# Optimization experiments

Measured on AMD Instinct MI355X. Metric: run time of the kernel, lower is better.

## Reference

```python
import jax, jax.numpy as jnp
import numpy as np

B, N, T, F, D, R, K, L, E = 4, 2000, 50, 10, 64, 8, 16, 3, 32


def setup_inputs() -> dict:
    key = jax.random.key(0)
    ks = jax.random.split(key, 12)
    rn = lambda k, shape, sc: (jax.random.normal(k, shape, jnp.float32) * sc)
    return {
        "X": jax.random.normal(ks[0], (B, N, T, F), jnp.float32),
        "neighbors": jax.random.randint(ks[1], (B, R, N, K), 0, N + 1),
        "gru_W": rn(ks[2], (F, 3 * D), 0.1),
        "gru_U": rn(ks[3], (D, 3 * D), 0.1),
        "gru_b": jnp.zeros((2, 3 * D), jnp.float32),
        "rel_emb": rn(ks[4], (R, E), 0.1),
        "proj_W": rn(ks[5], (R, D, D), 0.05),
        "proj_b": jnp.zeros((R, D), jnp.float32),
        "satt_W": rn(ks[6], (R, 2 * D + E), 0.05),
        "satt_b": jnp.zeros((R,), jnp.float32),
        "ratt_W": rn(ks[7], (2 * D + E,), 0.05),
        "ratt_b": jnp.zeros((), jnp.float32),
        "pred_W": rn(ks[8], (D, L), 0.05),
        "pred_b": jnp.zeros((L,), jnp.float32),
    }


def leaky(x):  # tf.nn.leaky_relu default alpha=0.2
    return jnp.where(x >= 0, x, 0.2 * x)


def gru(x, W, U, b):
    # Keras GRU (reset_after=True), gate order [z, r, h]. x: (M, T, F)
    xp = x @ W + b[0]                      # (M, T, 3D) input projections, precomputed
    h0 = jnp.zeros((x.shape[0], U.shape[0]), x.dtype)

    def step(h, xt):
        rec = h @ U + b[1]
        xz, xr, xh = jnp.split(xt, 3, axis=-1)
        rz, rr, rh = jnp.split(rec, 3, axis=-1)
        z = jax.nn.sigmoid(xz + rz)
        r = jax.nn.sigmoid(xr + rr)
        hh = jnp.tanh(xh + r * rh)
        return z * h + (1.0 - z) * hh, None

    h, _ = jax.lax.scan(step, h0, jnp.swapaxes(xp, 0, 1))
    return h


def reference(X, neighbors, gru_W, gru_U, gru_b, rel_emb, proj_W, proj_b,
              satt_W, satt_b, ratt_W, ratt_b, pred_W, pred_b):
    b, n, t, f = X.shape
    d = gru_U.shape[0]

    # --- GRU feature extraction (dropout inactive at inference) ---
    node = gru(X.reshape(b * n, t, f), gru_W, gru_U, gru_b).reshape(b, n, d)
    padded = jnp.concatenate([jnp.zeros((b, 1, d), node.dtype), node], axis=1)  # (B, N+1, D)

    # --- per-relation neighbor gather + projection ---
    neigh_raw = jax.vmap(lambda nf, idx: nf[idx])(padded, neighbors)            # (B, R, N, K, D)
    neigh = leaky(jnp.einsum('brnkd,rde->brnke', neigh_raw, proj_W)
                  + proj_b[None, :, None, None, :])                              # (B, R, N, K, D)

    cur = node                                                                   # (B, N, D)

    # --- state attention: Dense(1) on concat[cur, neigh, rel_emb], split weights ---
    w_cur, w_ngh, w_rel = satt_W[:, :d], satt_W[:, d:2 * d], satt_W[:, 2 * d:]
    s_cur = jnp.einsum('bnd,rd->brn', cur, w_cur)                                # (B, R, N)
    s_ngh = jnp.einsum('brnkd,rd->brnk', neigh, w_ngh)                           # (B, R, N, K)
    s_rel = jnp.einsum('re,re->r', rel_emb, w_rel) + satt_b                      # (R,)
    scores = leaky(s_cur[:, :, :, None] + s_ngh + s_rel[None, :, None, None])
    scores = scores + jnp.where(neighbors == 0, -1e9, 0.0).astype(scores.dtype)  # mask padding node
    att = jax.nn.softmax(scores, axis=-1)                                        # over K
    rel_rep = jnp.einsum('brnk,brnkd->brnd', att, neigh)                         # (B, R, N, D)

    # --- relation attention ---
    rep_t = jnp.transpose(rel_rep, (0, 2, 1, 3))                                 # (B, N, R, D)
    r_cur, r_rep, r_emb = ratt_W[:d], ratt_W[d:2 * d], ratt_W[2 * d:]
    rs = leaky(jnp.einsum('bnd,d->bn', cur, r_cur)[:, :, None]
               + jnp.einsum('bnrd,d->bnr', rep_t, r_rep)
               + (rel_emb @ r_emb)[None, None, :] + ratt_b)                      # (B, N, R)
    ratt = jax.nn.softmax(rs, axis=-1)
    agg = jnp.einsum('bnr,bnrd->bnd', ratt, rep_t)
    updated = cur + agg

    # --- prediction head ---
    return jax.nn.softmax(updated @ pred_W + pred_b)
```

## Files before the change

### kernel.cpp

```cpp
#include <hip/hip_runtime.h>
#include <hip/hip_bf16.h>
#include <cstddef>

constexpr int cB=4, cN=2000, cT=50, cF=10, cD=64, cR=8, cK=16, cE=32;
constexpr int NODES = cB*cN;
constexpr int N1    = cN+1;
constexpr int ROWS2 = cB*N1;

#define DEV static __device__ __forceinline__

typedef __attribute__((ext_vector_type(8))) short bf16x8;
typedef __attribute__((ext_vector_type(4))) float f32x4;
typedef __attribute__((ext_vector_type(4))) int   i32x4;

DEV float leaky(float x){ return fmaxf(x, 0.2f*x); }
DEV float wsumall(float v){
  v += __shfl_xor(v,32,64); v += __shfl_xor(v,16,64); v += __shfl_xor(v,8,64);
  v += __shfl_xor(v,4,64);  v += __shfl_xor(v,2,64);  v += __shfl_xor(v,1,64);
  return v;
}
DEV unsigned fu(float f){ return __float_as_uint(f); }
DEV float hif(float f){ return __uint_as_float(fu(f) & 0xFFFF0000u); }
DEV unsigned rne16(float f){
  unsigned u = fu(f);
  return (u + 0x7FFFu + ((u>>16)&1u)) >> 16;
}
DEV bf16x8 pack4(unsigned a, unsigned b, unsigned c2, unsigned d){
  union { i32x4 i; bf16x8 h; } u;
  u.i = (i32x4){(int)a,(int)b,(int)c2,(int)d};
  return u.h;
}
DEV unsigned PLO(unsigned x, unsigned y){ return __builtin_amdgcn_perm(y, x, 0x05040100u); }
DEV unsigned PHI(unsigned x, unsigned y){ return __builtin_amdgcn_perm(y, x, 0x07060302u); }
DEV f32x4 MF(bf16x8 a, bf16x8 b, f32x4 c){
  return __builtin_amdgcn_mfma_f32_16x16x32_bf16(a, b, c, 0, 0, 0);
}
DEV float bfu(unsigned short u){ return __uint_as_float(((unsigned)u)<<16); }

__global__ __launch_bounds__(256, 2) void k_gru(const float* __restrict__ X,
    const float* __restrict__ gW, const float* __restrict__ gU,
    const float* __restrict__ gb, const float* __restrict__ pW,
    const float* __restrict__ pb, const float* __restrict__ sattW,
    float* __restrict__ node, unsigned short* __restrict__ actb,
    float* __restrict__ sng2)
{
  __shared__ unsigned sH[2][1024];

  const int tid  = threadIdx.x;
  const int lane = tid & 63;
  const int w    = tid >> 6;
  const int c    = lane & 15;
  const int kg   = lane >> 4;
  const int nb   = (int)blockIdx.x * 16;
  const int col  = 16*w + c;
  const int bb   = nb / cN;

  bf16x8 BUhi[2][3], BUlo[2][3], BX[3];
  #pragma unroll
  for (int s=0;s<2;++s){
    #pragma unroll
    for (int cls=0; cls<3; ++cls){
      const int n = cls*64 + col;
      unsigned hi[4], lo[4];
      #pragma unroll
      for (int p=0;p<4;++p){
        float u0 = gU[(s*32 + kg*8 + 2*p    )*192 + n];
        float u1 = gU[(s*32 + kg*8 + 2*p + 1)*192 + n];
        hi[p] = (fu(u0)>>16) | (fu(u1) & 0xFFFF0000u);
        lo[p] = rne16(u0 - hif(u0)) | (rne16(u1 - hif(u1)) << 16);
      }
      BUhi[s][cls] = pack4(hi[0],hi[1],hi[2],hi[3]);
      BUlo[s][cls] = pack4(lo[0],lo[1],lo[2],lo[3]);
    }
  }
  #pragma unroll
  for (int cls=0; cls<3; ++cls){
    const int n = cls*64 + col;
    unsigned wd[4];
    #pragma unroll
    for (int p=0;p<4;++p){
      int f = kg*4 + p;
      unsigned v = (f < cF) ? rne16(gW[f*192 + n]) : 0u;
      wd[p] = v | (v << 16);
    }
    BX[cls] = pack4(wd[0],wd[1],wd[2],wd[3]);
  }

  const float bz  = gb[col]      + gb[192+col];
  const float br  = gb[64+col]   + gb[256+col];
  const float bh0 = gb[128+col];
  const float bh1 = gb[320+col];

  for (int i2 = tid; i2 < 1024; i2 += 256) sH[0][i2] = 0u;
  f32x4 ho = {0.f,0.f,0.f,0.f};
  __syncthreads();

  float xc[4], xn[4];
  const float* Xb = X + (size_t)(nb + c)*cT*cF;
  {
    #pragma unroll
    for (int p=0;p<4;++p){ int f = 4*kg+p; xc[p] = (f < cF) ? Xb[0*cF + f] : 0.f; }
    #pragma unroll
    for (int p=0;p<4;++p){ int f = 4*kg+p; xn[p] = (f < cF) ? Xb[1*cF + f] : 0.f; }
  }

  const unsigned sw  = (unsigned)((c&7)<<2);
  const unsigned rb0 = (unsigned)(c*64 + kg*8);

  for (int t = 0; t < cT; ++t){
    unsigned xw[4];
    #pragma unroll
    for (int p=0;p<4;++p)
      xw[p] = (fu(xc[p])>>16) | (rne16(xc[p] - hif(xc[p])) << 16);
    bf16x8 xf = pack4(xw[0],xw[1],xw[2],xw[3]);

    #pragma unroll
    for (int p=0;p<4;++p) xc[p] = xn[p];
    {
      int tn = (t+2 < cT) ? t+2 : cT-1;
      #pragma unroll
      for (int p=0;p<4;++p){ int f = 4*kg+p; xn[p] = (f < cF) ? Xb[(size_t)tn*cF + f] : 0.f; }
    }

    const unsigned* sr = sH[t & 1];
    i32x4 qa = *(const i32x4*)(sr + ((rb0 +  0) ^ sw));
    i32x4 qb = *(const i32x4*)(sr + ((rb0 +  4) ^ sw));
    i32x4 qc = *(const i32x4*)(sr + ((rb0 + 32) ^ sw));
    i32x4 qd = *(const i32x4*)(sr + ((rb0 + 36) ^ sw));
    bf16x8 hh0 = pack4(PLO(qa[0],qa[1]), PLO(qa[2],qa[3]), PLO(qb[0],qb[1]), PLO(qb[2],qb[3]));
    bf16x8 hl0 = pack4(PHI(qa[0],qa[1]), PHI(qa[2],qa[3]), PHI(qb[0],qb[1]), PHI(qb[2],qb[3]));
    bf16x8 hh1 = pack4(PLO(qc[0],qc[1]), PLO(qc[2],qc[3]), PLO(qd[0],qd[1]), PLO(qd[2],qd[3]));
    bf16x8 hl1 = pack4(PHI(qc[0],qc[1]), PHI(qc[2],qc[3]), PHI(qd[0],qd[1]), PHI(qd[2],qd[3]));

    f32x4 aZ  = {bz,bz,bz,bz};
    f32x4 aR  = {br,br,br,br};
    f32x4 aHc = {bh1,bh1,bh1,bh1};
    f32x4 aXh = {bh0,bh0,bh0,bh0};
    aZ  = MF(xf, BX[0], aZ);
    aR  = MF(xf, BX[1], aR);
    aXh = MF(xf, BX[2], aXh);
    aZ  = MF(hh0, BUhi[0][0], aZ);  aZ  = MF(hh1, BUhi[1][0], aZ);
    aR  = MF(hh0, BUhi[0][1], aR);  aR  = MF(hh1, BUhi[1][1], aR);
    aHc = MF(hh0, BUhi[0][2], aHc); aHc = MF(hh1, BUhi[1][2], aHc);
    aZ  = MF(hl0, BUhi[0][0], aZ);  aZ  = MF(hl1, BUhi[1][0], aZ);
    aR  = MF(hl0, BUhi[0][1], aR);  aR  = MF(hl1, BUhi[1][1], aR);
    aHc = MF(hl0, BUhi[0][2], aHc); aHc = MF(hl1, BUhi[1][2], aHc);
    aZ  = MF(hh0, BUlo[0][0], aZ);  aZ  = MF(hh1, BUlo[1][0], aZ);
    aR  = MF(hh0, BUlo[0][1], aR);  aR  = MF(hh1, BUlo[1][1], aR);
    aHc = MF(hh0, BUlo[0][2], aHc); aHc = MF(hh1, BUlo[1][2], aHc);

    unsigned* swr = sH[(t & 1) ^ 1];
    #pragma unroll
    for (int reg=0; reg<4; ++reg){
      float z  = __builtin_amdgcn_rcpf(1.0f + __expf(-aZ[reg]));
      float r  = __builtin_amdgcn_rcpf(1.0f + __expf(-aR[reg]));
      float pre = __builtin_fmaf(r, aHc[reg], aXh[reg]);
      float th = 1.0f - 2.0f*__builtin_amdgcn_rcpf(__expf(2.0f*pre) + 1.0f);
      float hn = __builtin_fmaf(z, ho[reg]-th, th);
      ho[reg] = hn;
      unsigned val = (fu(hn)>>16) | (rne16(hn - hif(hn)) << 16);
      int nodei = kg*4 + reg;
      swr[((unsigned)(nodei*64 + col)) ^ ((unsigned)((nodei&7)<<2))] = val;
    }
    asm volatile("s_waitcnt lgkmcnt(0)" ::: "memory");
    __builtin_amdgcn_s_barrier();
  }

  #pragma unroll
  for (int reg=0; reg<4; ++reg)
    node[(size_t)(nb + kg*4 + reg)*cD + col] = ho[reg];

  {
    const unsigned* sr = &sH[0][0];
    i32x4 qa = *(const i32x4*)(sr + ((rb0 +  0) ^ sw));
    i32x4 qb = *(const i32x4*)(sr + ((rb0 +  4) ^ sw));
    i32x4 qc = *(const i32x4*)(sr + ((rb0 + 32) ^ sw));
    i32x4 qd = *(const i32x4*)(sr + ((rb0 + 36) ^ sw));
    bf16x8 hh0 = pack4(PLO(qa[0],qa[1]), PLO(qa[2],qa[3]), PLO(qb[0],qb[1]), PLO(qb[2],qb[3]));
    bf16x8 hl0 = pack4(PHI(qa[0],qa[1]), PHI(qa[2],qa[3]), PHI(qb[0],qb[1]), PHI(qb[2],qb[3]));
    bf16x8 hh1 = pack4(PLO(qc[0],qc[1]), PLO(qc[2],qc[3]), PLO(qd[0],qd[1]), PLO(qd[2],qd[3]));
    bf16x8 hl1 = pack4(PHI(qc[0],qc[1]), PHI(qc[2],qc[3]), PHI(qd[0],qd[1]), PHI(qd[2],qd[3]));

    const int qbase = nb + bb + 1;
    #pragma unroll
    for (int r2=0; r2<2; ++r2){
      const int r = 2*w + r2;
      const float* Pr = pW + (size_t)r*cD*cD;
      bf16x8 PB[4][2];
      float pbv[4], wnv[4];
      #pragma unroll
      for (int cb=0; cb<4; ++cb){
        const int e = 16*cb + c;
        #pragma unroll
        for (int s=0;s<2;++s){
          unsigned wd[4];
          #pragma unroll
          for (int p=0;p<4;++p){
            int k0 = s*32 + kg*8 + 2*p;
            wd[p] = rne16(Pr[(size_t)k0*cD + e]) | (rne16(Pr[(size_t)(k0+1)*cD + e]) << 16);
          }
          PB[cb][s] = pack4(wd[0],wd[1],wd[2],wd[3]);
        }
        pbv[cb] = pb[r*cD + e];
        wnv[cb] = sattW[r*(2*cD+cE) + cD + e];
      }
      float sp[4] = {0.f,0.f,0.f,0.f};
      #pragma unroll
      for (int cb=0; cb<4; ++cb){
        f32x4 acc = {pbv[cb],pbv[cb],pbv[cb],pbv[cb]};
        acc = MF(hh0, PB[cb][0], acc); acc = MF(hh1, PB[cb][1], acc);
        acc = MF(hl0, PB[cb][0], acc); acc = MF(hl1, PB[cb][1], acc);
        #pragma unroll
        for (int reg=0; reg<4; ++reg){
          float o = leaky(acc[reg]);
          int qrow = qbase + kg*4 + reg;
          actb[((size_t)r*ROWS2 + qrow)*cD + 16*cb + c] = (unsigned short)rne16(o);
          sp[reg] = __builtin_fmaf(o, wnv[cb], sp[reg]);
        }
      }
      #pragma unroll
      for (int reg=0; reg<4; ++reg){
        float s2 = sp[reg];
        s2 += __shfl_xor(s2,1,64); s2 += __shfl_xor(s2,2,64);
        s2 += __shfl_xor(s2,4,64); s2 += __shfl_xor(s2,8,64);
        if (c == 0) sng2[(size_t)r*ROWS2 + qbase + kg*4 + reg] = s2;
      }
    }
  }

  if ((blockIdx.x % (cN/16)) == 0){
    #pragma unroll
    for (int r2=0; r2<2; ++r2){
      const int r = 2*w + r2;
      float v0 = leaky(pb[r*cD + lane]);
      float wv = sattW[r*(2*cD+cE) + cD + lane];
      actb[((size_t)r*ROWS2 + (size_t)bb*N1)*cD + lane] = (unsigned short)rne16(v0);
      float s2 = wsumall(v0 * wv);
      if (lane == 0) sng2[(size_t)r*ROWS2 + (size_t)bb*N1] = s2;
    }
  }
}

__global__ __launch_bounds__(256) void k_attn(const float* __restrict__ node,
    const int* __restrict__ nbrs, const float* __restrict__ sattW,
    const float* __restrict__ sattb, const float* __restrict__ rattW,
    const float* __restrict__ rattb, const float* __restrict__ predW,
    const float* __restrict__ predb, const float* __restrict__ relemb,
    const unsigned short* __restrict__ actb, const float* __restrict__ sng2,
    float* __restrict__ out)
{
  __shared__ float sSA[cR][cD];
  __shared__ float sSrel[cR], sRremb[cR];
  __shared__ float sAtt[4][cR][cK];
  __shared__ int   sOff[4][cR][cK];
  const int tid = threadIdx.x;
  for (int i=tid; i<cR*cD; i+=256) sSA[i>>6][i&63] = sattW[(i>>6)*(2*cD+cE) + (i&63)];
  if (tid < 64){
    int r = tid >> 3, j0 = (tid & 7)*4;
    float a = 0.f, b2 = 0.f;
    #pragma unroll
    for (int j=0;j<4;++j){
      float re = relemb[r*cE + j0 + j];
      a  += re * sattW[r*(2*cD+cE) + 2*cD + j0 + j];
      b2 += re * rattW[2*cD + j0 + j];
    }
    a  += __shfl_xor(a,1,64);  a  += __shfl_xor(a,2,64);  a  += __shfl_xor(a,4,64);
    b2 += __shfl_xor(b2,1,64); b2 += __shfl_xor(b2,2,64); b2 += __shfl_xor(b2,4,64);
    if ((tid & 7) == 0){ sSrel[r] = a + sattb[r]; sRremb[r] = b2; }
  }
  __syncthreads();

  const int wave = tid >> 6, lane = tid & 63;
  const int gn = (int)blockIdx.x*4 + wave;
  const int b = __builtin_amdgcn_readfirstlane(gn / cN);
  const int n = __builtin_amdgcn_readfirstlane(gn % cN);

  const float cur = node[(size_t)gn*cD + lane];

  float scr[8];
  #pragma unroll
  for (int r=0; r<8; ++r) scr[r] = wsumall(cur * sSA[r][lane]);

  const int g = lane >> 4, k = lane & 15;
  #pragma unroll
  for (int half=0; half<2; ++half){
    int r = half*4 + g;
    float sc0 = half==0 ? (g==0?scr[0]:g==1?scr[1]:g==2?scr[2]:scr[3])
                        : (g==0?scr[4]:g==1?scr[5]:g==2?scr[6]:scr[7]);
    int idx = nbrs[(((size_t)b*cR + r)*cN + n)*cK + k];
    int o = r*ROWS2 + b*N1 + idx;
    float sv = sng2[o];
    float sc = leaky(sc0 + sv + sSrel[r]);
    if (idx == 0) sc -= 1e9f;
    float mx = sc;
    mx = fmaxf(mx, __shfl_xor(mx,1,64)); mx = fmaxf(mx, __shfl_xor(mx,2,64));
    mx = fmaxf(mx, __shfl_xor(mx,4,64)); mx = fmaxf(mx, __shfl_xor(mx,8,64));
    float ex = __expf(sc - mx);
    float sm = ex;
    sm += __shfl_xor(sm,1,64); sm += __shfl_xor(sm,2,64);
    sm += __shfl_xor(sm,4,64); sm += __shfl_xor(sm,8,64);
    sAtt[wave][r][k] = ex/sm;
    sOff[wave][r][k] = o;
  }
  __syncthreads();

  float facc[8];
  #pragma unroll
  for (int r=0; r<8; ++r){
    float a0=0.f, a1=0.f;
    #pragma unroll
    for (int kk=0; kk<cK; kk+=2){
      float w0 = sAtt[wave][r][kk],   w1 = sAtt[wave][r][kk+1];
      int   o0 = sOff[wave][r][kk],   o1 = sOff[wave][r][kk+1];
      a0 += w0 * bfu(actb[(size_t)o0*cD + lane]);
      a1 += w1 * bfu(actb[(size_t)o1*cD + lane]);
    }
    facc[r] = a0 + a1;
  }

  const float rcur = rattW[lane], rrep = rattW[cD + lane];
  const float rb   = rattb[0];
  const float c0 = wsumall(cur * rcur);
  float rs[8];
  #pragma unroll
  for (int r=0; r<8; ++r) rs[r] = leaky(c0 + wsumall(facc[r]*rrep) + sRremb[r] + rb);
  float mx = rs[0];
  #pragma unroll
  for (int r=1; r<8; ++r) mx = fmaxf(mx, rs[r]);
  float es = 0.f; float ratt[8];
  #pragma unroll
  for (int r=0; r<8; ++r){ ratt[r] = __expf(rs[r]-mx); es += ratt[r]; }
  float inv = 1.f/es;
  float agg = 0.f;
  #pragma unroll
  for (int r=0; r<8; ++r) agg += (ratt[r]*inv) * facc[r];
  const float upd = cur + agg;

  float l0 = wsumall(upd * predW[lane*3 + 0]);
  float l1 = wsumall(upd * predW[lane*3 + 1]);
  float l2 = wsumall(upd * predW[lane*3 + 2]);
  if (lane == 0){
    l0 += predb[0]; l1 += predb[1]; l2 += predb[2];
    float m2 = fmaxf(l0, fmaxf(l1, l2));
    float e0 = __expf(l0-m2), e1 = __expf(l1-m2), e2 = __expf(l2-m2);
    float is = 1.f/(e0+e1+e2);
    out[(size_t)gn*3+0] = e0*is;
    out[(size_t)gn*3+1] = e1*is;
    out[(size_t)gn*3+2] = e2*is;
  }
}

extern "C" void kernel_launch(void* const* d_in, const int* in_sizes, int n_in,
                              void* d_out, int out_size, void* d_ws, size_t ws_size,
                              hipStream_t stream)
{
  const float* X      = (const float*)d_in[0];
  const int*   nbrs   = (const int*)  d_in[1];
  const float* gW     = (const float*)d_in[2];
  const float* gU     = (const float*)d_in[3];
  const float* gb     = (const float*)d_in[4];
  const float* relemb = (const float*)d_in[5];
  const float* pW     = (const float*)d_in[6];
  const float* pb     = (const float*)d_in[7];
  const float* sattW  = (const float*)d_in[8];
  const float* sattb  = (const float*)d_in[9];
  const float* rattW  = (const float*)d_in[10];
  const float* rattb  = (const float*)d_in[11];
  const float* predW  = (const float*)d_in[12];
  const float* predb  = (const float*)d_in[13];
  float* out = (float*)d_out;

  float*          node  = (float*)d_ws;
  unsigned short* actb  = (unsigned short*)(node + (size_t)NODES*cD);
  float*          sng2  = (float*)(actb + (size_t)cR*ROWS2*cD);

  k_gru <<<NODES/16, 256, 0, stream>>>(X, gW, gU, gb, pW, pb, sattW,
                                       node, actb, sng2);
  k_attn<<<NODES/4, 256, 0, stream>>>(node, nbrs, sattW, sattb, rattW, rattb,
                                      predW, predb, relemb, actb, sng2, out);
}
```

Baseline: 88.80 us.

## Switch GRU recurrence from split-bf16 MFMA to single fp16 MFMA with folded scales

Replaces the three-pass split-bf16 (hi/lo) recurrent matmul with a single fp16 MFMA per tile. The weights are prescaled by -log2(e) and 2*log2(e) so the sigmoid and tanh can use a raw v_exp_f32, and the input bias is folded into the input MFMA through a constant-1 feature slot. The hidden state shared-memory buffer is halved and the permute/unpack work is removed. This cuts MFMA count and ALU work on the serial 50-step critical path, at the cost of fp16 precision in the hidden state and weights, which could exceed the accuracy tolerance.

```diff
diff --git a/kernel.cpp b/kernel.cpp
--- a/kernel.cpp
+++ b/kernel.cpp
@@ -1,6 +1,7 @@
 #include <hip/hip_runtime.h>
 #include <hip/hip_bf16.h>
 #include <cstddef>
+#include <cstring>
 
 constexpr int cB=4, cN=2000, cT=50, cF=10, cD=64, cR=8, cK=16, cE=32;
 constexpr int NODES = cB*cN;
@@ -9,9 +10,10 @@
 
 #define DEV static __device__ __forceinline__
 
-typedef __attribute__((ext_vector_type(8))) short bf16x8;
-typedef __attribute__((ext_vector_type(4))) float f32x4;
-typedef __attribute__((ext_vector_type(4))) int   i32x4;
+typedef __attribute__((ext_vector_type(8))) short    bf16x8;
+typedef __attribute__((ext_vector_type(8))) _Float16 f16x8;
+typedef __attribute__((ext_vector_type(4))) float    f32x4;
+typedef __attribute__((ext_vector_type(4))) int      i32x4;
 
 DEV float leaky(float x){ return fmaxf(x, 0.2f*x); }
 DEV float wsumall(float v){
@@ -20,22 +22,28 @@
   return v;
 }
 DEV unsigned fu(float f){ return __float_as_uint(f); }
-DEV float hif(float f){ return __uint_as_float(fu(f) & 0xFFFF0000u); }
 DEV unsigned rne16(float f){
   unsigned u = fu(f);
   return (u + 0x7FFFu + ((u>>16)&1u)) >> 16;
 }
-DEV bf16x8 pack4(unsigned a, unsigned b, unsigned c2, unsigned d){
-  union { i32x4 i; bf16x8 h; } u;
+DEV unsigned f16b(float f){
+  _Float16 h = (_Float16)f;
+  unsigned short u; __builtin_memcpy(&u, &h, 2);
+  return (unsigned)u;
+}
+DEV f16x8 packh(unsigned a, unsigned b, unsigned c2, unsigned d){
+  union { i32x4 i; f16x8 h; } u;
   u.i = (i32x4){(int)a,(int)b,(int)c2,(int)d};
   return u.h;
 }
-DEV unsigned PLO(unsigned x, unsigned y){ return __builtin_amdgcn_perm(y, x, 0x05040100u); }
-DEV unsigned PHI(unsigned x, unsigned y){ return __builtin_amdgcn_perm(y, x, 0x07060302u); }
-DEV f32x4 MF(bf16x8 a, bf16x8 b, f32x4 c){
-  return __builtin_amdgcn_mfma_f32_16x16x32_bf16(a, b, c, 0, 0, 0);
+DEV f16x8 asf16(i32x4 v){
+  union { i32x4 i; f16x8 h; } u; u.i = v; return u.h;
+}
+DEV f32x4 MF16(f16x8 a, f16x8 b, f32x4 c){
+  return __builtin_amdgcn_mfma_f32_16x16x32_f16(a, b, c, 0, 0, 0);
 }
 DEV float bfu(unsigned short u){ return __uint_as_float(((unsigned)u)<<16); }
+DEV float ex2(float x){ float r; asm("v_exp_f32 %0, %1" : "=v"(r) : "v"(x)); return r; }
 
 __global__ __launch_bounds__(256, 2) void k_gru(const float* __restrict__ X,
     const float* __restrict__ gW, const float* __restrict__ gU,
@@ -44,7 +52,7 @@
     float* __restrict__ node, unsigned short* __restrict__ actb,
     float* __restrict__ sng2)
 {
-  __shared__ unsigned sH[2][1024];
+  __shared__ unsigned sF[2][512];
 
   const int tid  = threadIdx.x;
   const int lane = tid & 63;
@@ -55,112 +63,108 @@
   const int col  = 16*w + c;
   const int bb   = nb / cN;
 
-  bf16x8 BUhi[2][3], BUlo[2][3], BX[3];
+  const float SZ = -1.4426950408889634f;
+  const float SH =  2.8853900817779268f;
+
+  f16x8 Uf[2][3];
   #pragma unroll
   for (int s=0;s<2;++s){
     #pragma unroll
     for (int cls=0; cls<3; ++cls){
+      const float sc = (cls==2) ? SH : SZ;
       const int n = cls*64 + col;
-      unsigned hi[4], lo[4];
+      unsigned wd[4];
       #pragma unroll
       for (int p=0;p<4;++p){
-        float u0 = gU[(s*32 + kg*8 + 2*p    )*192 + n];
-        float u1 = gU[(s*32 + kg*8 + 2*p + 1)*192 + n];
-        hi[p] = (fu(u0)>>16) | (fu(u1) & 0xFFFF0000u);
-        lo[p] = rne16(u0 - hif(u0)) | (rne16(u1 - hif(u1)) << 16);
-      }
-      BUhi[s][cls] = pack4(hi[0],hi[1],hi[2],hi[3]);
-      BUlo[s][cls] = pack4(lo[0],lo[1],lo[2],lo[3]);
-    }
-  }
+        int d0 = s*32 + kg*8 + 2*p;
+        wd[p] = f16b(sc*gU[d0*192 + n]) | (f16b(sc*gU[(d0+1)*192 + n]) << 16);
+      }
+      Uf[s][cls] = packh(wd[0],wd[1],wd[2],wd[3]);
+    }
+  }
+  const float bzt = SZ*(gb[col] + gb[192+col]);
+  const float brt = SZ*(gb[64+col] + gb[256+col]);
+  const float bh0 = SH* gb[128+col];
+  const float bh1 = SH* gb[320+col];
+  f16x8 BXf[3];
   #pragma unroll
   for (int cls=0; cls<3; ++cls){
+    const float sc = (cls==2) ? SH : SZ;
+    const float bv = (cls==0) ? bzt : (cls==1 ? brt : bh0);
     const int n = cls*64 + col;
     unsigned wd[4];
     #pragma unroll
     for (int p=0;p<4;++p){
       int f = kg*4 + p;
-      unsigned v = (f < cF) ? rne16(gW[f*192 + n]) : 0u;
-      wd[p] = v | (v << 16);
-    }
-    BX[cls] = pack4(wd[0],wd[1],wd[2],wd[3]);
-  }
-
-  const float bz  = gb[col]      + gb[192+col];
-  const float br  = gb[64+col]   + gb[256+col];
-  const float bh0 = gb[128+col];
-  const float bh1 = gb[320+col];
-
-  for (int i2 = tid; i2 < 1024; i2 += 256) sH[0][i2] = 0u;
+      unsigned v = (f < cF) ? f16b(sc*gW[f*192 + n]) : ((f == cF) ? f16b(bv) : 0u);
+      wd[p] = v;
+    }
+    BXf[cls] = packh(wd[0],wd[1],wd[2],wd[3]);
+  }
+
+  for (int i2 = tid; i2 < 512; i2 += 256) sF[0][i2] = 0u;
   f32x4 ho = {0.f,0.f,0.f,0.f};
   __syncthreads();
 
   float xc[4], xn[4];
   const float* Xb = X + (size_t)(nb + c)*cT*cF;
-  {
-    #pragma unroll
-    for (int p=0;p<4;++p){ int f = 4*kg+p; xc[p] = (f < cF) ? Xb[0*cF + f] : 0.f; }
-    #pragma unroll
-    for (int p=0;p<4;++p){ int f = 4*kg+p; xn[p] = (f < cF) ? Xb[1*cF + f] : 0.f; }
-  }
-
-  const unsigned sw  = (unsigned)((c&7)<<2);
-  const unsigned rb0 = (unsigned)(c*64 + kg*8);
+  #pragma unroll
+  for (int p=0;p<4;++p){
+    int f = 4*kg+p;
+    float fill = (f == cF) ? 1.0f : 0.0f;
+    xc[p] = (f < cF) ? Xb[0*cF + f] : fill;
+    xn[p] = (f < cF) ? Xb[1*cF + f] : fill;
+  }
+
+  const unsigned sw2   = (unsigned)((c&7)<<2);
+  const unsigned base0 = ((unsigned)(c*32 + kg*4))      ^ sw2;
+  const unsigned base1 = ((unsigned)(c*32 + 16 + kg*4)) ^ sw2;
+  unsigned hws[4];
+  #pragma unroll
+  for (int reg=0; reg<4; ++reg){
+    int nodei = kg*4 + reg;
+    hws[reg] = (((unsigned)(nodei*32 + (col>>1))) ^ ((unsigned)((nodei&7)<<2)))*2
+               + (unsigned)(col&1);
+  }
+  const f32x4 zq = {0.f,0.f,0.f,0.f};
 
   for (int t = 0; t < cT; ++t){
-    unsigned xw[4];
-    #pragma unroll
-    for (int p=0;p<4;++p)
-      xw[p] = (fu(xc[p])>>16) | (rne16(xc[p] - hif(xc[p])) << 16);
-    bf16x8 xf = pack4(xw[0],xw[1],xw[2],xw[3]);
-
+    f16x8 xf = packh(f16b(xc[0]), f16b(xc[1]), f16b(xc[2]), f16b(xc[3]));
     #pragma unroll
     for (int p=0;p<4;++p) xc[p] = xn[p];
     {
       int tn = (t+2 < cT) ? t+2 : cT-1;
       #pragma unroll
-      for (int p=0;p<4;++p){ int f = 4*kg+p; xn[p] = (f < cF) ? Xb[(size_t)tn*cF + f] : 0.f; }
-    }
-
-    const unsigned* sr = sH[t & 1];
-    i32x4 qa = *(const i32x4*)(sr + ((rb0 +  0) ^ sw));
-    i32x4 qb = *(const i32x4*)(sr + ((rb0 +  4) ^ sw));
-    i32x4 qc = *(const i32x4*)(sr + ((rb0 + 32) ^ sw));
-    i32x4 qd = *(const i32x4*)(sr + ((rb0 + 36) ^ sw));
-    bf16x8 hh0 = pack4(PLO(qa[0],qa[1]), PLO(qa[2],qa[3]), PLO(qb[0],qb[1]), PLO(qb[2],qb[3]));
-    bf16x8 hl0 = pack4(PHI(qa[0],qa[1]), PHI(qa[2],qa[3]), PHI(qb[0],qb[1]), PHI(qb[2],qb[3]));
-    bf16x8 hh1 = pack4(PLO(qc[0],qc[1]), PLO(qc[2],qc[3]), PLO(qd[0],qd[1]), PLO(qd[2],qd[3]));
-    bf16x8 hl1 = pack4(PHI(qc[0],qc[1]), PHI(qc[2],qc[3]), PHI(qd[0],qd[1]), PHI(qd[2],qd[3]));
-
-    f32x4 aZ  = {bz,bz,bz,bz};
-    f32x4 aR  = {br,br,br,br};
+      for (int p=0;p<4;++p){
+        int f = 4*kg+p;
+        float fill = (f == cF) ? 1.0f : 0.0f;
+        xn[p] = (f < cF) ? Xb[(size_t)tn*cF + f] : fill;
+      }
+    }
+
+    const unsigned* sr = sF[t & 1];
+    i32x4 q0 = *(const i32x4*)(sr + base0);
+    i32x4 q1 = *(const i32x4*)(sr + base1);
+    f16x8 ha = asf16(q0), hb = asf16(q1);
+
+    f32x4 aZ  = MF16(xf, BXf[0], zq);
+    f32x4 aR  = MF16(xf, BXf[1], zq);
+    f32x4 aXh = MF16(xf, BXf[2], zq);
     f32x4 aHc = {bh1,bh1,bh1,bh1};
-    f32x4 aXh = {bh0,bh0,bh0,bh0};
-    aZ  = MF(xf, BX[0], aZ);
-    aR  = MF(xf, BX[1], aR);
-    aXh = MF(xf, BX[2], aXh);
-    aZ  = MF(hh0, BUhi[0][0], aZ);  aZ  = MF(hh1, BUhi[1][0], aZ);
-    aR  = MF(hh0, BUhi[0][1], aR);  aR  = MF(hh1, BUhi[1][1], aR);
-    aHc = MF(hh0, BUhi[0][2], aHc); aHc = MF(hh1, BUhi[1][2], aHc);
-    aZ  = MF(hl0, BUhi[0][0], aZ);  aZ  = MF(hl1, BUhi[1][0], aZ);
-    aR  = MF(hl0, BUhi[0][1], aR);  aR  = MF(hl1, BUhi[1][1], aR);
-    aHc = MF(hl0, BUhi[0][2], aHc); aHc = MF(hl1, BUhi[1][2], aHc);
-    aZ  = MF(hh0, BUlo[0][0], aZ);  aZ  = MF(hh1, BUlo[1][0], aZ);
-    aR  = MF(hh0, BUlo[0][1], aR);  aR  = MF(hh1, BUlo[1][1], aR);
-    aHc = MF(hh0, BUlo[0][2], aHc); aHc = MF(hh1, BUlo[1][2], aHc);
-
-    unsigned* swr = sH[(t & 1) ^ 1];
+    aZ  = MF16(ha, Uf[0][0], aZ);  aZ  = MF16(hb, Uf[1][0], aZ);
+    aR  = MF16(ha, Uf[0][1], aR);  aR  = MF16(hb, Uf[1][1], aR);
+    aHc = MF16(ha, Uf[0][2], aHc); aHc = MF16(hb, Uf[1][2], aHc);
+
+    unsigned short* swr = (unsigned short*)sF[(t & 1) ^ 1];
     #pragma unroll
     for (int reg=0; reg<4; ++reg){
-      float z  = __builtin_amdgcn_rcpf(1.0f + __expf(-aZ[reg]));
-      float r  = __builtin_amdgcn_rcpf(1.0f + __expf(-aR[reg]));
-      float pre = __builtin_fmaf(r, aHc[reg], aXh[reg]);
-      float th = 1.0f - 2.0f*__builtin_amdgcn_rcpf(__expf(2.0f*pre) + 1.0f);
-      float hn = __builtin_fmaf(z, ho[reg]-th, th);
+      float z   = __builtin_amdgcn_rcpf(1.0f + ex2(aZ[reg]));
+      float r   = __builtin_amdgcn_rcpf(1.0f + ex2(aR[reg]));
+      float phv = __builtin_fmaf(r, aHc[reg], aXh[reg]);
+      float th  = __builtin_fmaf(-2.0f, __builtin_amdgcn_rcpf(ex2(phv) + 1.0f), 1.0f);
+      float hn  = __builtin_fmaf(z, ho[reg]-th, th);
       ho[reg] = hn;
-      unsigned val = (fu(hn)>>16) | (rne16(hn - hif(hn)) << 16);
-      int nodei = kg*4 + reg;
-      swr[((unsigned)(nodei*64 + col)) ^ ((unsigned)((nodei&7)<<2))] = val;
+      swr[hws[reg]] = (unsigned short)f16b(hn);
     }
     asm volatile("s_waitcnt lgkmcnt(0)" ::: "memory");
     __builtin_amdgcn_s_barrier();
@@ -171,35 +175,30 @@
     node[(size_t)(nb + kg*4 + reg)*cD + col] = ho[reg];
 
   {
-    const unsigned* sr = &sH[0][0];
-    i32x4 qa = *(const i32x4*)(sr + ((rb0 +  0) ^ sw));
-    i32x4 qb = *(const i32x4*)(sr + ((rb0 +  4) ^ sw));
-    i32x4 qc = *(const i32x4*)(sr + ((rb0 + 32) ^ sw));
-    i32x4 qd = *(const i32x4*)(sr + ((rb0 + 36) ^ sw));
-    bf16x8 hh0 = pack4(PLO(qa[0],qa[1]), PLO(qa[2],qa[3]), PLO(qb[0],qb[1]), PLO(qb[2],qb[3]));
-    bf16x8 hl0 = pack4(PHI(qa[0],qa[1]), PHI(qa[2],qa[3]), PHI(qb[0],qb[1]), PHI(qb[2],qb[3]));
-    bf16x8 hh1 = pack4(PLO(qc[0],qc[1]), PLO(qc[2],qc[3]), PLO(qd[0],qd[1]), PLO(qd[2],qd[3]));
-    bf16x8 hl1 = pack4(PHI(qc[0],qc[1]), PHI(qc[2],qc[3]), PHI(qd[0],qd[1]), PHI(qd[2],qd[3]));
+    const unsigned* sr = &sF[0][0];
+    i32x4 q0 = *(const i32x4*)(sr + base0);
+    i32x4 q1 = *(const i32x4*)(sr + base1);
+    f16x8 ha = asf16(q0), hb = asf16(q1);
 
     const int qbase = nb + bb + 1;
     #pragma unroll
-    for (int r2=0; r2<2; ++r2){
-      const int r = 2*w + r2;
+    for (int rr=0; rr<2; ++rr){
+      const int r = 2*w + rr;
       const float* Pr = pW + (size_t)r*cD*cD;
-      bf16x8 PB[4][2];
+      f16x8 PB[4][2];
       float pbv[4], wnv[4];
       #pragma unroll
       for (int cb=0; cb<4; ++cb){
         const int e = 16*cb + c;
         #pragma unroll
-        for (int s=0;s<2;++s){
+        for (int s2=0;s2<2;++s2){
           unsigned wd[4];
           #pragma unroll
           for (int p=0;p<4;++p){
-            int k0 = s*32 + kg*8 + 2*p;
-            wd[p] = rne16(Pr[(size_t)k0*cD + e]) | (rne16(Pr[(size_t)(k0+1)*cD + e]) << 16);
+            int d0 = s2*32 + kg*8 + 2*p;
+            wd[p] = f16b(Pr[(size_t)d0*cD + e]) | (f16b(Pr[(size_t)(d0+1)*cD + e]) << 16);
           }
-          PB[cb][s] = pack4(wd[0],wd[1],wd[2],wd[3]);
+          PB[cb][s2] = packh(wd[0],wd[1],wd[2],wd[3]);
         }
         pbv[cb] = pb[r*cD + e];
         wnv[cb] = sattW[r*(2*cD+cE) + cD + e];
@@ -208,8 +207,8 @@
       #pragma unroll
       for (int cb=0; cb<4; ++cb){
         f32x4 acc = {pbv[cb],pbv[cb],pbv[cb],pbv[cb]};
-        acc = MF(hh0, PB[cb][0], acc); acc = MF(hh1, PB[cb][1], acc);
-        acc = MF(hl0, PB[cb][0], acc); acc = MF(hl1, PB[cb][1], acc);
+        acc = MF16(ha, PB[cb][0], acc);
+        acc = MF16(hb, PB[cb][1], acc);
         #pragma unroll
         for (int reg=0; reg<4; ++reg){
           float o = leaky(acc[reg]);
@@ -230,8 +229,8 @@
 
   if ((blockIdx.x % (cN/16)) == 0){
     #pragma unroll
-    for (int r2=0; r2<2; ++r2){
-      const int r = 2*w + r2;
+    for (int rr=0; rr<2; ++rr){
+      const int r = 2*w + rr;
       float v0 = leaky(pb[r*cD + lane]);
       float wv = sattW[r*(2*cD+cE) + cD + lane];
       actb[((size_t)r*ROWS2 + (size_t)bb*N1)*cD + lane] = (unsigned short)rne16(v0);
```

New measurement: 81.03 us. 1.1x faster.
